# Kernel optimization log

Measured on AMD Instinct MI355X. Metric: run time of the kernel, lower is better.

Reference implementation:

```python
import jax, jax.numpy as jnp
import numpy as np

H, DK, DIM, DFF, DEPTH = 8, 64, 512, 2048, 8
B, LS, LT, VOCAB = 16, 128, 128, 32000


def setup_inputs() -> dict:
    key = jax.random.key(0)
    ks = jax.random.split(key, 20)
    w = lambda k, s: jax.random.normal(k, s, jnp.float32) * 0.02
    N_enc, N_dec = B * LS, B * LT
    base_s = np.arange(B) * LS
    base_t = np.arange(B) * LT
    i = np.arange(LS)
    j = np.arange(LT)
    # encoder self-attn: full bipartite within each sentence
    ee_src = (base_s[:, None, None] + i[None, :, None] + 0 * i[None, None, :]).reshape(-1)
    ee_dst = (base_s[:, None, None] + 0 * i[None, :, None] + i[None, None, :]).reshape(-1)
    # decoder self-attn: causal (key pos <= query pos)
    ii, jj = np.meshgrid(j, j, indexing='ij')  # ii = dst(query) pos, jj = src(key) pos
    m = jj <= ii
    dd_src = (base_t[:, None] + jj[m][None, :]).reshape(-1)
    dd_dst = (base_t[:, None] + ii[m][None, :]).reshape(-1)
    # cross-attn: enc node -> dec node, full within sentence
    ed_src = (base_s[:, None, None] + i[None, :, None] + 0 * j[None, None, :]).reshape(-1)
    ed_dst = (base_t[:, None, None] + 0 * i[None, :, None] + j[None, None, :]).reshape(-1)
    return {
        'emb_src': w(ks[0], (VOCAB, DIM)), 'emb_tgt': w(ks[1], (VOCAB, DIM)),
        'pos_emb': w(ks[2], (LS, DIM)), 'time_emb': w(ks[3], (DEPTH, DIM)),
        'Wqkv_e': w(ks[4], (DIM, 3 * DIM)), 'Wo_e': w(ks[5], (DIM, DIM)),
        'W1_e': w(ks[6], (DIM, DFF)), 'W2_e': w(ks[7], (DFF, DIM)),
        'Wqkv_d': w(ks[8], (DIM, 3 * DIM)), 'Wo_d': w(ks[9], (DIM, DIM)),
        'W1_d': w(ks[10], (DIM, DFF)), 'W2_d': w(ks[11], (DFF, DIM)),
        'Wq_x': w(ks[12], (DIM, DIM)), 'Wkv_x': w(ks[13], (DIM, 2 * DIM)),
        'Wo_x': w(ks[14], (DIM, DIM)), 'Wgen': w(ks[15], (DIM, VOCAB)),
        'src_tokens': jax.random.randint(ks[16], (N_enc,), 0, VOCAB, jnp.int32),
        'tgt_tokens': jax.random.randint(ks[17], (N_dec,), 0, VOCAB, jnp.int32),
        'src_pos': jnp.tile(jnp.arange(LS, dtype=jnp.int32), B),
        'tgt_pos': jnp.tile(jnp.arange(LT, dtype=jnp.int32), B),
        'ee_src': jnp.asarray(ee_src, jnp.int32), 'ee_dst': jnp.asarray(ee_dst, jnp.int32),
        'dd_src': jnp.asarray(dd_src, jnp.int32), 'dd_dst': jnp.asarray(dd_dst, jnp.int32),
        'ed_src': jnp.asarray(ed_src, jnp.int32), 'ed_dst': jnp.asarray(ed_dst, jnp.int32),
    }


def _ln(x):
    m = x.mean(-1, keepdims=True)
    v = ((x - m) ** 2).mean(-1, keepdims=True)
    return (x - m) * jax.lax.rsqrt(v + 1e-5)


def _attn(q, k, v, src, dst, n_dst):
    # q: [Nq,H,DK] (dst side), k/v: [Nk,H,DK] (src side); edge lists [E]
    # src_dot_dst -> scaled_exp -> scatter-sum (src_mul_edge + sum, copy_edge + sum), then wv/z
    s = jnp.exp(jnp.einsum('ehd,ehd->eh', k[src], q[dst]) / np.float32(np.sqrt(DK)))  # [E,H]
    wv = jax.ops.segment_sum(s[:, :, None] * v[src], dst, num_segments=n_dst)  # [Nq,H,DK]
    z = jax.ops.segment_sum(s, dst, num_segments=n_dst)  # [Nq,H]
    return (wv / (z[:, :, None] + 1e-9)).reshape(n_dst, DIM)


def reference(emb_src, emb_tgt, pos_emb, time_emb, Wqkv_e, Wo_e, W1_e, W2_e,
              Wqkv_d, Wo_d, W1_d, W2_d, Wq_x, Wkv_x, Wo_x, Wgen,
              src_tokens, tgt_tokens, src_pos, tgt_pos,
              ee_src, ee_dst, dd_src, dd_dst, ed_src, ed_dst):
    Ne, Nd = src_tokens.shape[0], tgt_tokens.shape[0]
    x_e = emb_src[src_tokens] + pos_emb[src_pos]
    x_d = emb_tgt[tgt_tokens] + pos_emb[tgt_pos]
    # encoder: MAX_DEPTH shared-weight iterations with time+pos enc re-added each step
    for t in range(DEPTH):
        xp = x_e + pos_emb[src_pos] + time_emb[t]
        q, k, v = jnp.split(xp @ Wqkv_e, 3, axis=-1)
        o = _attn(q.reshape(Ne, H, DK), k.reshape(Ne, H, DK), v.reshape(Ne, H, DK), ee_src, ee_dst, Ne)
        x_e = _ln(x_e + o @ Wo_e)
        x_e = _ln(x_e + jax.nn.relu(x_e @ W1_e) @ W2_e)
    # decoder: self-attn (causal dd) then cross-attn (ed) each iteration
    for t in range(DEPTH):
        xp = x_d + pos_emb[tgt_pos] + time_emb[t]
        q, k, v = jnp.split(xp @ Wqkv_d, 3, axis=-1)
        o = _attn(q.reshape(Nd, H, DK), k.reshape(Nd, H, DK), v.reshape(Nd, H, DK), dd_src, dd_dst, Nd)
        x_d = _ln(x_d + o @ Wo_d)
        qx = ((x_d + pos_emb[tgt_pos] + time_emb[t]) @ Wq_x).reshape(Nd, H, DK)
        kx, vx = jnp.split(x_e @ Wkv_x, 2, axis=-1)
        o = _attn(qx, kx.reshape(Ne, H, DK), vx.reshape(Ne, H, DK), ed_src, ed_dst, Nd)
        x_d = _ln(x_d + o @ Wo_x)
        x_d = _ln(x_d + jax.nn.relu(x_d @ W1_d) @ W2_d)
    return jax.nn.log_softmax(x_d @ Wgen, axis=-1)  # generator over dec nodes
```

## Files before the change

kernel.cpp:

```cpp
#include <hip/hip_runtime.h>
#include <hip/hip_bf16.h>
#include <math.h>

#define H 8
#define DK 64
#define DIM 512
#define DFF 2048
#define DEPTH 8
#define VOCAB 32000
#define NTOK 2048

typedef float f32x4 __attribute__((ext_vector_type(4)));
typedef short bf16x8 __attribute__((ext_vector_type(8)));

static __device__ __forceinline__ unsigned short f2bf(float f) {
    unsigned u = __float_as_uint(f);
    return (unsigned short)((u + 0x7FFFu + ((u >> 16) & 1u)) >> 16);
}

#define GLL(src, dst) __builtin_amdgcn_global_load_lds( \
    (const __attribute__((address_space(1))) unsigned int*)(src), \
    (__attribute__((address_space(3))) unsigned int*)(dst), 16, 0, 0)

static __device__ __forceinline__ void load_ln_stats(
    const float* __restrict__ stats, int base, int rows,
    float* Lm, float* Li, int tid, int nthr)
{
    for (int r = tid; r < rows; r += nthr) {
        float m = 0.f, inv = 1.f;
        if (stats) {
            const float* s = stats + (size_t)(base + r) * 16;
            float sum = 0.f, sq = 0.f;
#pragma unroll
            for (int b = 0; b < 8; b++) { sum += s[b * 2]; sq += s[b * 2 + 1]; }
            m = sum * (1.f / 512.f);
            float v = sq * (1.f / 512.f) - m * m;
            inv = 1.f / sqrtf(v + 1e-5f);
        }
        Lm[r] = m; Li[r] = inv;
    }
}

__global__ void embed_kernel(const float* __restrict__ emb, const int* __restrict__ tok,
                             const float* __restrict__ pos, const int* __restrict__ pidx,
                             float* __restrict__ out, int n4) {
    int idx = blockIdx.x * blockDim.x + threadIdx.x;
    if (idx >= n4) return;
    int i = idx >> 7, d = idx & 127;
    float4 a = ((const float4*)emb)[(size_t)tok[i] * 128 + d];
    float4 b = ((const float4*)pos)[(size_t)pidx[i] * 128 + d];
    ((float4*)out)[idx] = make_float4(a.x + b.x, a.y + b.y, a.z + b.z, a.w + b.w);
}

struct WD { const float* src; unsigned short* dst; int K; int N; int t0; int pad; };
struct WTab { WD d[12]; };

__global__ __launch_bounds__(256) void wconv_all(WTab tab) {
    __shared__ float t[32][33];
    const int bid = blockIdx.x;
    int w = 0;
#pragma unroll
    for (int i = 1; i < 12; i++) if (bid >= tab.d[i].t0) w = i;
    const float* W = tab.d[w].src;
    unsigned short* Wt = tab.d[w].dst;
    const int K = tab.d[w].K, N = tab.d[w].N;
    const int lt = bid - tab.d[w].t0;
    const int txc = N >> 5;
    const int n0 = (lt % txc) << 5, k0 = (lt / txc) << 5;
    const int tid = threadIdx.x;
    const int tx = tid & 31, ty = tid >> 5;
#pragma unroll
    for (int i = 0; i < 32; i += 8)
        t[ty + i][tx] = W[(size_t)(k0 + ty + i) * N + n0 + tx];
    __syncthreads();
#pragma unroll
    for (int i = 0; i < 32; i += 8)
        Wt[(size_t)(n0 + ty + i) * K + k0 + tx] = f2bf(t[tx][ty + i]);
}

template<int EPI>
__global__ __launch_bounds__(256) void gemm_rb(
    const float* __restrict__ Tf,
    const float* __restrict__ stats,
    const unsigned short* __restrict__ Bt,
    unsigned short* __restrict__ Cb,
    int M, int N, int K)
{
    constexpr int BN = 64, JN = 2;
    __shared__ __align__(16) unsigned short Asm[2][128 * 64];
    __shared__ __align__(16) unsigned short Bsm[2][BN * 64];
    __shared__ float Lm[128], Li[128];
    const int tid = threadIdx.x;
    const int lane = tid & 63, wid = tid >> 6;
    const int m0 = blockIdx.y * 128, n0 = blockIdx.x * BN;
    const int wm = (wid >> 1) * 64, wn = (wid & 1) * (BN / 2);
    const int NK = K >> 6;

    float4 ar0[4], ar1[4];
    auto loadA = [&](int k0) {
#pragma unroll
        for (int it = 0; it < 4; it++) {
            int q = it * 256 + tid;
            int row = q >> 3;
            int cs = q & 7;
            const float* s = Tf + (size_t)(m0 + row) * K + k0 + cs * 8;
            ar0[it] = *(const float4*)s;
            ar1[it] = *(const float4*)(s + 4);
        }
    };
    auto storeA = [&](int buf) {
#pragma unroll
        for (int it = 0; it < 4; it++) {
            int q = it * 256 + tid;
            int row = q >> 3;
            int cs = q & 7;
            float m = Lm[row], iv = Li[row];
            unsigned short c8[8];
            c8[0] = f2bf((ar0[it].x - m) * iv); c8[1] = f2bf((ar0[it].y - m) * iv);
            c8[2] = f2bf((ar0[it].z - m) * iv); c8[3] = f2bf((ar0[it].w - m) * iv);
            c8[4] = f2bf((ar1[it].x - m) * iv); c8[5] = f2bf((ar1[it].y - m) * iv);
            c8[6] = f2bf((ar1[it].z - m) * iv); c8[7] = f2bf((ar1[it].w - m) * iv);
            *(bf16x8*)&Asm[buf][row * 64 + ((cs ^ (row & 7)) * 8)] = *(bf16x8*)c8;
        }
    };
    auto stageB = [&](int k0, int buf) {
#pragma unroll
        for (int it = 0; it < BN / 32; it++) {
            int q = it * 256 + tid;
            int row = q >> 3;
            int cs = (q & 7) ^ (row & 7);
            GLL(Bt + (size_t)(n0 + row) * K + k0 + cs * 8, &Bsm[buf][q * 8]);
        }
    };

    load_ln_stats(stats, m0, 128, Lm, Li, tid, 256);
    loadA(0);
    __syncthreads();
    storeA(0);
    stageB(0, 0);

    f32x4 acc[4][JN];
#pragma unroll
    for (int i = 0; i < 4; i++)
#pragma unroll
        for (int j = 0; j < JN; j++) acc[i][j] = (f32x4){0.f, 0.f, 0.f, 0.f};

    for (int kt = 0; kt < NK; kt++) {
        __syncthreads();
        const int cur = kt & 1, nxt = (kt + 1) & 1;
        if (kt + 1 < NK) {
            stageB((kt + 1) << 6, nxt);
            loadA((kt + 1) << 6);
        }
#pragma unroll
        for (int kk = 0; kk < 2; kk++) {
            bf16x8 af[4], bfr[JN];
#pragma unroll
            for (int i = 0; i < 4; i++) {
                int rowA = wm + i * 16 + (lane & 15);
                int ca = (kk * 4 + (lane >> 4)) ^ (rowA & 7);
                af[i] = *(const bf16x8*)&Asm[cur][rowA * 64 + ca * 8];
            }
#pragma unroll
            for (int j = 0; j < JN; j++) {
                int rowB = wn + j * 16 + (lane & 15);
                int cb = (kk * 4 + (lane >> 4)) ^ (rowB & 7);
                bfr[j] = *(const bf16x8*)&Bsm[cur][rowB * 64 + cb * 8];
            }
#pragma unroll
            for (int i = 0; i < 4; i++)
#pragma unroll
                for (int j = 0; j < JN; j++)
                    acc[i][j] = __builtin_amdgcn_mfma_f32_16x16x32_bf16(af[i], bfr[j], acc[i][j], 0, 0, 0);
        }
        if (kt + 1 < NK) storeA(nxt);
    }
#pragma unroll
    for (int i = 0; i < 4; i++)
#pragma unroll
        for (int j = 0; j < JN; j++)
#pragma unroll
            for (int r = 0; r < 4; r++) {
                int row = m0 + wm + i * 16 + (lane >> 4) * 4 + r;
                int col = n0 + wn + j * 16 + (lane & 15);
                size_t idx = (size_t)row * N + col;
                float v = acc[i][j][r];
                if (EPI == 1) Cb[idx] = f2bf(fmaxf(v, 0.f));
                if (EPI == 3) Cb[idx] = f2bf(v);
            }
}

__global__ __launch_bounds__(256) void gemm_bb(
    const unsigned short* __restrict__ A,
    const unsigned short* __restrict__ Bt,
    const float* __restrict__ Tin,
    const float* __restrict__ statsIn,
    float* __restrict__ Tout,
    float* __restrict__ statsOut,
    int M, int K)
{
    __shared__ __align__(16) unsigned short Asm[2][32 * 64];
    __shared__ __align__(16) unsigned short Bsm[2][64 * 64];
    __shared__ float Lm[32], Li[32];
    __shared__ float sredS[4][32], sredQ[4][32];
    const int tid = threadIdx.x;
    const int lane = tid & 63, wid = tid >> 6;
    const int nb = blockIdx.x;
    const int m0 = blockIdx.y * 32, n0 = nb * 64;
    const int wn = wid * 16;
    const int NK = K >> 6;

    auto stage = [&](int k0, int buf) {
        {
            int q = tid;
            int row = q >> 3;
            int cs = (q & 7) ^ (row & 7);
            GLL(A + (size_t)(m0 + row) * K + k0 + cs * 8, &Asm[buf][q * 8]);
        }
#pragma unroll
        for (int it = 0; it < 2; it++) {
            int q = it * 256 + tid;
            int row = q >> 3;
            int cs = (q & 7) ^ (row & 7);
            GLL(Bt + (size_t)(n0 + row) * K + k0 + cs * 8, &Bsm[buf][q * 8]);
        }
    };

    load_ln_stats(statsIn, m0, 32, Lm, Li, tid, 256);
    stage(0, 0);

    f32x4 acc[2];
#pragma unroll
    for (int i = 0; i < 2; i++) acc[i] = (f32x4){0.f, 0.f, 0.f, 0.f};

    for (int kt = 0; kt < NK; kt++) {
        __syncthreads();
        const int cur = kt & 1, nxt = (kt + 1) & 1;
        if (kt + 1 < NK) stage((kt + 1) << 6, nxt);
#pragma unroll
        for (int kd = 0; kd < 2; kd++) {
            int rowB = wn + (lane & 15);
            int cb = (kd * 4 + (lane >> 4)) ^ (rowB & 7);
            bf16x8 bfr = *(const bf16x8*)&Bsm[cur][rowB * 64 + cb * 8];
#pragma unroll
            for (int i = 0; i < 2; i++) {
                int rowA = i * 16 + (lane & 15);
                int ca = (kd * 4 + (lane >> 4)) ^ (rowA & 7);
                bf16x8 af = *(const bf16x8*)&Asm[cur][rowA * 64 + ca * 8];
                acc[i] = __builtin_amdgcn_mfma_f32_16x16x32_bf16(af, bfr, acc[i], 0, 0, 0);
            }
        }
    }
#pragma unroll
    for (int i = 0; i < 2; i++) {
#pragma unroll
        for (int r = 0; r < 4; r++) {
            int rl = i * 16 + (lane >> 4) * 4 + r;
            int row = m0 + rl;
            int col = n0 + wn + (lane & 15);
            size_t idx = (size_t)row * DIM + col;
            float rv = (Tin[idx] - Lm[rl]) * Li[rl];
            float v = acc[i][r] + rv;
            Tout[idx] = v;
            float s = v, q = v * v;
            s += __shfl_xor(s, 1); s += __shfl_xor(s, 2);
            s += __shfl_xor(s, 4); s += __shfl_xor(s, 8);
            q += __shfl_xor(q, 1); q += __shfl_xor(q, 2);
            q += __shfl_xor(q, 4); q += __shfl_xor(q, 8);
            if ((lane & 15) == 0) { sredS[wid][rl] = s; sredQ[wid][rl] = q; }
        }
    }
    __syncthreads();
    if (tid < 32) {
        int row = tid;
        float s = sredS[0][row] + sredS[1][row] + sredS[2][row] + sredS[3][row];
        float q = sredQ[0][row] + sredQ[1][row] + sredQ[2][row] + sredQ[3][row];
        statsOut[(size_t)(m0 + row) * 16 + nb * 2] = s;
        statsOut[(size_t)(m0 + row) * 16 + nb * 2 + 1] = q;
    }
}

template<int CAUSAL>
static __device__ __forceinline__ void attn_phase2_split(
    const unsigned short* Qs, const unsigned short* Ks, const unsigned short* Vt,
    unsigned short* Psw, float* dumpf,
    int qh, int wid, int lane, int tok0, int h,
    unsigned short* __restrict__ O)
{
    const int qg = wid & 3, kh = wid >> 2;
    bf16x8 qa[2];
#pragma unroll
    for (int kd = 0; kd < 2; kd++) {
        int qr = qg * 16 + (lane & 15);
        int ch = (kd * 4 + (lane >> 4)) ^ (qr & 7);
        qa[kd] = *(const bf16x8*)&Qs[qr * 64 + ch * 8];
    }
    int jn, kcn;
    if (!CAUSAL)      { jn = 4; kcn = 2; }
    else if (kh > qh) { jn = 0; kcn = 0; }
    else if (kh < qh) { jn = 4; kcn = 2; }
    else              { kcn = (qg >> 1) + 1; jn = kcn * 2; }

    float zr[4] = {0.f, 0.f, 0.f, 0.f};
    f32x4 oacc[4];
#pragma unroll
    for (int dt = 0; dt < 4; dt++) oacc[dt] = (f32x4){0.f, 0.f, 0.f, 0.f};

    if (jn > 0) {
        f32x4 sacc[4];
#pragma unroll
        for (int j = 0; j < 4; j++) sacc[j] = (f32x4){0.f, 0.f, 0.f, 0.f};
#pragma unroll 2
        for (int kd = 0; kd < 2; kd++) {
            for (int jj = 0; jj < jn; jj++) {
                int kr = kh * 64 + jj * 16 + (lane & 15);
                int ch = (kd * 4 + (lane >> 4)) ^ (kr & 7);
                bf16x8 kf = *(const bf16x8*)&Ks[kr * 64 + ch * 8];
                sacc[jj] = __builtin_amdgcn_mfma_f32_16x16x32_bf16(qa[kd], kf, sacc[jj], 0, 0, 0);
            }
        }
        int qbase = qh * 64 + qg * 16 + (lane >> 4) * 4;
        for (int jj = 0; jj < jn; jj++) {
            int kcol = kh * 64 + jj * 16 + (lane & 15);
#pragma unroll
            for (int rr = 0; rr < 4; rr++) {
                float p = __expf(sacc[jj][rr] * 0.125f);
                if (CAUSAL && kcol > qbase + rr) p = 0.f;
                zr[rr] += p;
                int prow = (lane >> 4) * 4 + rr;
                int ch = ((jj * 2 + ((lane & 15) >> 3)) ^ (prow & 7));
                Psw[prow * 64 + ch * 8 + (lane & 7)] = f2bf(p);
            }
        }
        for (int kcl = 0; kcl < kcn; kcl++) {
            bf16x8 pa;
            {
                int prow = lane & 15;
                int ch = (kcl * 4 + (lane >> 4)) ^ (prow & 7);
                pa = *(const bf16x8*)&Psw[prow * 64 + ch * 8];
            }
            int kcg = kh * 2 + kcl;
#pragma unroll
            for (int dt = 0; dt < 4; dt++) {
                int d = dt * 16 + (lane & 15);
                bf16x8 vf = *(const bf16x8*)&Vt[d * 132 + (kcg * 4 + (lane >> 4)) * 8];
                oacc[dt] = __builtin_amdgcn_mfma_f32_16x16x32_bf16(pa, vf, oacc[dt], 0, 0, 0);
            }
        }
    }
    __syncthreads();
    if (kh == 1) {
        float* dst = dumpf + (size_t)(qg * 64 + lane) * 20;
#pragma unroll
        for (int dt = 0; dt < 4; dt++)
#pragma unroll
            for (int rr = 0; rr < 4; rr++) dst[dt * 4 + rr] = oacc[dt][rr];
#pragma unroll
        for (int rr = 0; rr < 4; rr++) dst[16 + rr] = zr[rr];
    }
    __syncthreads();
    if (kh == 0) {
        const float* src = dumpf + (size_t)(qg * 64 + lane) * 20;
#pragma unroll
        for (int dt = 0; dt < 4; dt++)
#pragma unroll
            for (int rr = 0; rr < 4; rr++) oacc[dt][rr] += src[dt * 4 + rr];
#pragma unroll
        for (int rr = 0; rr < 4; rr++) {
            float z = zr[rr] + src[16 + rr];
            z += __shfl_xor(z, 1); z += __shfl_xor(z, 2);
            z += __shfl_xor(z, 4); z += __shfl_xor(z, 8);
            zr[rr] = 1.f / (z + 1e-9f);
        }
#pragma unroll
        for (int dt = 0; dt < 4; dt++)
#pragma unroll
            for (int rr = 0; rr < 4; rr++) {
                int qrow = tok0 + qh * 64 + qg * 16 + (lane >> 4) * 4 + rr;
                O[(size_t)qrow * DIM + h * 64 + dt * 16 + (lane & 15)] =
                    f2bf(oacc[dt][rr] * zr[rr]);
            }
    }
}

template<int CAUSAL>
__global__ __launch_bounds__(512) void fused_attn(
    const float* __restrict__ Tf,
    const float* __restrict__ stats,
    const float* __restrict__ pos,
    const float* __restrict__ trow,
    const unsigned short* __restrict__ WqkvT,
    unsigned short* __restrict__ O)
{
    __shared__ __align__(16) unsigned short smem[28928];
    __shared__ float LmA[128], LiA[128];
    unsigned short* Asm = smem;
    unsigned short* Bsm = smem + 8192;
    unsigned short* Qs  = smem;
    unsigned short* Ks  = smem + 4096;
    unsigned short* Vt  = smem + 12288;
    float* dumpf = (float*)smem;
    const int tid = threadIdx.x;
    const int lane = tid & 63, wid = tid >> 6;
    unsigned short* Psw = smem + 20736 + wid * 1024;
    const int blk = blockIdx.x;
    const int qh = blk & 1, h = (blk >> 1) & 7, b = blk >> 4;
    const int tok0 = b * 128;
    const int wr = wid * 16;

    load_ln_stats(stats, tok0, 128, LmA, LiA, tid, 512);
    __syncthreads();

    f32x4 acc[12];
#pragma unroll
    for (int c = 0; c < 12; c++) acc[c] = (f32x4){0.f, 0.f, 0.f, 0.f};

    for (int k0 = 0; k0 < 512; k0 += 64) {
        if (k0) __syncthreads();
#pragma unroll
        for (int it = 0; it < 3; it++) {
            int q = it * 512 + wid * 64 + lane;
            int r = q >> 3;
            int cs = (q & 7) ^ (r & 7);
            int srow = (r < 64) ? (h * 64 + r)
                     : (r < 128) ? (512 + h * 64 + (r - 64))
                                 : (1024 + h * 64 + (r - 128));
            GLL(WqkvT + (size_t)srow * 512 + k0 + cs * 8, &Bsm[(it * 512 + wid * 64) * 8]);
        }
#pragma unroll
        for (int it = 0; it < 2; it++) {
            int q = it * 512 + tid;
            int row = q >> 3;
            int cs = q & 7;
            const float* s = Tf + (size_t)(tok0 + row) * 512 + k0 + cs * 8;
            const float* pp = pos + (size_t)row * 512 + k0 + cs * 8;
            const float* tt = trow + k0 + cs * 8;
            float4 u0 = *(const float4*)s, u1 = *(const float4*)(s + 4);
            float4 p0 = *(const float4*)pp, p1 = *(const float4*)(pp + 4);
            float4 t0 = *(const float4*)tt, t1 = *(const float4*)(tt + 4);
            float m = LmA[row], iv = LiA[row];
            unsigned short c8[8];
            c8[0] = f2bf((u0.x - m) * iv + p0.x + t0.x);
            c8[1] = f2bf((u0.y - m) * iv + p0.y + t0.y);
            c8[2] = f2bf((u0.z - m) * iv + p0.z + t0.z);
            c8[3] = f2bf((u0.w - m) * iv + p0.w + t0.w);
            c8[4] = f2bf((u1.x - m) * iv + p1.x + t1.x);
            c8[5] = f2bf((u1.y - m) * iv + p1.y + t1.y);
            c8[6] = f2bf((u1.z - m) * iv + p1.z + t1.z);
            c8[7] = f2bf((u1.w - m) * iv + p1.w + t1.w);
            *(bf16x8*)&Asm[row * 64 + ((cs ^ (row & 7)) * 8)] = *(bf16x8*)c8;
        }
        __syncthreads();
#pragma unroll
        for (int kk = 0; kk < 2; kk++) {
            int rowA = wr + (lane & 15);
            int ca = (kk * 4 + (lane >> 4)) ^ (rowA & 7);
            bf16x8 af = *(const bf16x8*)&Asm[rowA * 64 + ca * 8];
#pragma unroll
            for (int c = 0; c < 12; c++) {
                int rowB = c * 16 + (lane & 15);
                int cb = (kk * 4 + (lane >> 4)) ^ (rowB & 7);
                bf16x8 bfr = *(const bf16x8*)&Bsm[rowB * 64 + cb * 8];
                acc[c] = __builtin_amdgcn_mfma_f32_16x16x32_bf16(af, bfr, acc[c], 0, 0, 0);
            }
        }
    }
    __syncthreads();
#pragma unroll
    for (int c = 0; c < 12; c++)
#pragma unroll
        for (int r = 0; r < 4; r++) {
            int token = wr + (lane >> 4) * 4 + r;
            int col = (c & 3) * 16 + (lane & 15);
            unsigned short v = f2bf(acc[c][r]);
            if (c < 4) {
                int tl = token - qh * 64;
                if (tl >= 0 && tl < 64)
                    Qs[tl * 64 + (((col >> 3) ^ (tl & 7)) * 8) + (col & 7)] = v;
            } else if (c < 8) {
                Ks[token * 64 + (((col >> 3) ^ (token & 7)) * 8) + (col & 7)] = v;
            } else {
                Vt[col * 132 + token] = v;
            }
        }
    __syncthreads();
    attn_phase2_split<CAUSAL>(Qs, Ks, Vt, Psw, dumpf, qh, wid, lane, tok0, h, O);
}

__global__ __launch_bounds__(512) void fused_xattn(
    const float* __restrict__ Tf,
    const float* __restrict__ stats,
    const float* __restrict__ pos,
    const float* __restrict__ trow,
    const unsigned short* __restrict__ WqT,
    const unsigned short* __restrict__ kvx,
    unsigned short* __restrict__ O)
{
    __shared__ __align__(16) unsigned short smem[28928];
    __shared__ float LmA[64], LiA[64];
    unsigned short* Qs  = smem;
    unsigned short* Ks  = smem + 4096;
    unsigned short* Vt  = smem + 12288;
    unsigned short* Asm = smem + 20736;
    unsigned short* Bsm = smem + 24832;
    float* dumpf = (float*)smem;
    const int tid = threadIdx.x;
    const int lane = tid & 63, wid = tid >> 6;
    unsigned short* Psw = smem + 20736 + wid * 1024;
    const int blk = blockIdx.x;
    const int qh = blk & 1, h = (blk >> 1) & 7, b = blk >> 4;
    const int tok0 = b * 128;

    load_ln_stats(stats, tok0 + qh * 64, 64, LmA, LiA, tid, 512);

    if (wid >= 4) {
        int st = tid - 256;
        int r = st >> 1, c0 = (st & 1) * 4;
        const unsigned short* Kg = kvx + (size_t)(tok0 + r) * 1024 + h * 64;
        const unsigned short* Vg = Kg + 512;
#pragma unroll
        for (int c = c0; c < c0 + 4; c++) {
            bf16x8 kv = *(const bf16x8*)&Kg[c * 8];
            *(bf16x8*)&Ks[r * 64 + ((c ^ (r & 7)) * 8)] = kv;
            bf16x8 vv = *(const bf16x8*)&Vg[c * 8];
#pragma unroll
            for (int j = 0; j < 8; j++)
                Vt[(c * 8 + j) * 132 + r] = (unsigned short)vv[j];
        }
    }
    __syncthreads();

    f32x4 acc[4];
#pragma unroll
    for (int c = 0; c < 4; c++) acc[c] = (f32x4){0.f, 0.f, 0.f, 0.f};

    for (int k0 = 0; k0 < 512; k0 += 64) {
        if (k0) __syncthreads();
        if (tid < 256) {
#pragma unroll
            for (int it = 0; it < 2; it++) {
                int q = it * 256 + tid;
                int r = q >> 3;
                int cs = (q & 7) ^ (r & 7);
                GLL(WqT + (size_t)(h * 64 + r) * 512 + k0 + cs * 8, &Bsm[q * 8]);
            }
#pragma unroll
            for (int it = 0; it < 2; it++) {
                int q = it * 256 + tid;
                int row = q >> 3;
                int cs = q & 7;
                const float* s = Tf + (size_t)(tok0 + qh * 64 + row) * 512 + k0 + cs * 8;
                const float* pp = pos + (size_t)(qh * 64 + row) * 512 + k0 + cs * 8;
                const float* tt = trow + k0 + cs * 8;
                float4 u0 = *(const float4*)s, u1 = *(const float4*)(s + 4);
                float4 p0 = *(const float4*)pp, p1 = *(const float4*)(pp + 4);
                float4 t0 = *(const float4*)tt, t1 = *(const float4*)(tt + 4);
                float m = LmA[row], iv = LiA[row];
                unsigned short c8[8];
                c8[0] = f2bf((u0.x - m) * iv + p0.x + t0.x);
                c8[1] = f2bf((u0.y - m) * iv + p0.y + t0.y);
                c8[2] = f2bf((u0.z - m) * iv + p0.z + t0.z);
                c8[3] = f2bf((u0.w - m) * iv + p0.w + t0.w);
                c8[4] = f2bf((u1.x - m) * iv + p1.x + t1.x);
                c8[5] = f2bf((u1.y - m) * iv + p1.y + t1.y);
                c8[6] = f2bf((u1.z - m) * iv + p1.z + t1.z);
                c8[7] = f2bf((u1.w - m) * iv + p1.w + t1.w);
                *(bf16x8*)&Asm[row * 64 + ((cs ^ (row & 7)) * 8)] = *(bf16x8*)c8;
            }
        }
        __syncthreads();
        if (wid < 4) {
#pragma unroll
            for (int kk = 0; kk < 2; kk++) {
                int rowA = wid * 16 + (lane & 15);
                int ca = (kk * 4 + (lane >> 4)) ^ (rowA & 7);
                bf16x8 af = *(const bf16x8*)&Asm[rowA * 64 + ca * 8];
#pragma unroll
                for (int c = 0; c < 4; c++) {
                    int rowB = c * 16 + (lane & 15);
                    int cb = (kk * 4 + (lane >> 4)) ^ (rowB & 7);
                    bf16x8 bfr = *(const bf16x8*)&Bsm[rowB * 64 + cb * 8];
                    acc[c] = __builtin_amdgcn_mfma_f32_16x16x32_bf16(af, bfr, acc[c], 0, 0, 0);
                }
            }
        }
    }
    __syncthreads();
    if (wid < 4) {
#pragma unroll
        for (int c = 0; c < 4; c++)
#pragma unroll
            for (int r = 0; r < 4; r++) {
                int tl = wid * 16 + (lane >> 4) * 4 + r;
                int col = c * 16 + (lane & 15);
                Qs[tl * 64 + (((col >> 3) ^ (tl & 7)) * 8) + (col & 7)] = f2bf(acc[c][r]);
            }
    }
    __syncthreads();
    attn_phase2_split<0>(Qs, Ks, Vt, Psw, dumpf, qh, wid, lane, tok0, h, O);
}

__global__ __launch_bounds__(64) void ln_fin(const float* __restrict__ T,
                                             const float* __restrict__ stats,
                                             unsigned short* __restrict__ outb) {
    const int row = blockIdx.x, lane = threadIdx.x;
    const float* st = stats + (size_t)row * 16;
    float sum = 0.f, sq = 0.f;
#pragma unroll
    for (int b = 0; b < 8; b++) { sum += st[b * 2]; sq += st[b * 2 + 1]; }
    float m = sum * (1.f / 512.f);
    float v = sq * (1.f / 512.f) - m * m;
    float inv = 1.f / sqrtf(v + 1e-5f);
    const float* p = T + (size_t)row * DIM;
    unsigned short* qb = outb + (size_t)row * DIM;
#pragma unroll
    for (int i = 0; i < 8; i++)
        qb[lane + i * 64] = f2bf((p[lane + i * 64] - m) * inv);
}

template<int PASS>
__global__ __launch_bounds__(512) void gemm_gen(
    const unsigned short* __restrict__ Ab,
    const unsigned short* __restrict__ Bt,
    float* __restrict__ Out,
    float* __restrict__ pm,
    float* __restrict__ psum,
    const float* __restrict__ lse)
{
    __shared__ __align__(16) unsigned short Asm[256 * 64];
    __shared__ __align__(16) unsigned short Bsm[128 * 64];
    __shared__ float pml[8][64];
    __shared__ float psl[8][64];
    __shared__ float lsh[256];
    const int tid = threadIdx.x;
    const int lane = tid & 63, wid = tid >> 6;
    const int d = blockIdx.x + blockIdx.y * 8;
    const int t = (d & 7) * 250 + (d >> 3);
    const int mt = t & 7, nt = t >> 3;
    const int m0 = mt * 256, n0 = nt * 128;
    const int wm = (wid >> 1) * 64, wn = (wid & 1) * 64;

    if (PASS == 1) {
        for (int r = tid; r < 256; r += 512) lsh[r] = lse[m0 + r];
        __syncthreads();
    }

    f32x4 acc[4][4];
#pragma unroll
    for (int i = 0; i < 4; i++)
#pragma unroll
        for (int j = 0; j < 4; j++) acc[i][j] = (f32x4){0.f, 0.f, 0.f, 0.f};

    for (int k0 = 0; k0 < 512; k0 += 64) {
        if (k0 || PASS == 1) __syncthreads();
#pragma unroll
        for (int it = 0; it < 2; it++) {
            int q = it * 512 + tid;
            int row = q >> 3;
            int cs = (q & 7) ^ (row & 7);
            GLL(Bt + (size_t)(n0 + row) * 512 + k0 + cs * 8, &Bsm[(it * 512 + wid * 64) * 8]);
        }
#pragma unroll
        for (int it = 0; it < 4; it++) {
            int q = it * 512 + tid;
            int row = q >> 3;
            int cs = (q & 7) ^ (row & 7);
            GLL(Ab + (size_t)(m0 + row) * 512 + k0 + cs * 8, &Asm[(it * 512 + wid * 64) * 8]);
        }
        __syncthreads();
#pragma unroll
        for (int kk = 0; kk < 2; kk++) {
            bf16x8 af[4], bfr[4];
#pragma unroll
            for (int i = 0; i < 4; i++) {
                int rowA = wm + i * 16 + (lane & 15);
                int ca = (kk * 4 + (lane >> 4)) ^ (rowA & 7);
                af[i] = *(const bf16x8*)&Asm[rowA * 64 + ca * 8];
                int rowB = wn + i * 16 + (lane & 15);
                int cb = (kk * 4 + (lane >> 4)) ^ (rowB & 7);
                bfr[i] = *(const bf16x8*)&Bsm[rowB * 64 + cb * 8];
            }
#pragma unroll
            for (int i = 0; i < 4; i++)
#pragma unroll
                for (int j = 0; j < 4; j++)
                    acc[i][j] = __builtin_amdgcn_mfma_f32_16x16x32_bf16(af[i], bfr[j], acc[i][j], 0, 0, 0);
        }
    }
    if (PASS == 0) {
#pragma unroll
        for (int i = 0; i < 4; i++) {
#pragma unroll
            for (int r = 0; r < 4; r++) {
                float mx = fmaxf(fmaxf(acc[i][0][r], acc[i][1][r]),
                                 fmaxf(acc[i][2][r], acc[i][3][r]));
                mx = fmaxf(mx, __shfl_xor(mx, 1));
                mx = fmaxf(mx, __shfl_xor(mx, 2));
                mx = fmaxf(mx, __shfl_xor(mx, 4));
                mx = fmaxf(mx, __shfl_xor(mx, 8));
                float s = __expf(acc[i][0][r] - mx) + __expf(acc[i][1][r] - mx) +
                          __expf(acc[i][2][r] - mx) + __expf(acc[i][3][r] - mx);
                s += __shfl_xor(s, 1); s += __shfl_xor(s, 2);
                s += __shfl_xor(s, 4); s += __shfl_xor(s, 8);
                if ((lane & 15) == 0) {
                    int li = i * 16 + (lane >> 4) * 4 + r;
                    pml[wid][li] = mx;
                    psl[wid][li] = s;
                }
            }
        }
        __syncthreads();
        if (tid < 256) {
            int g = tid >> 6, lr = tid & 63;
            int wa = g * 2, wb = g * 2 + 1;
            float m = fmaxf(pml[wa][lr], pml[wb][lr]);
            float s = psl[wa][lr] * __expf(pml[wa][lr] - m) + psl[wb][lr] * __expf(pml[wb][lr] - m);
            pm[(size_t)(m0 + g * 64 + lr) * 256 + nt] = m;
            psum[(size_t)(m0 + g * 64 + lr) * 256 + nt] = s;
        }
    } else {
#pragma unroll
        for (int i = 0; i < 4; i++)
#pragma unroll
            for (int j = 0; j < 4; j++)
#pragma unroll
                for (int r = 0; r < 4; r++) {
                    int rl = wm + i * 16 + (lane >> 4) * 4 + r;
                    int col = n0 + wn + j * 16 + (lane & 15);
                    Out[(size_t)(m0 + rl) * VOCAB + col] = acc[i][j][r] - lsh[rl];
                }
    }
}

__global__ __launch_bounds__(64) void lse_kernel(const float* __restrict__ pm,
                                                 const float* __restrict__ psum,
                                                 float* __restrict__ lse) {
    const int row = blockIdx.x, t = threadIdx.x;
    float m = -1e30f, s = 0.f;
    for (int nb = t; nb < 250; nb += 64) {
        float mm = pm[(size_t)row * 256 + nb];
        float ss = psum[(size_t)row * 256 + nb];
        float M = fmaxf(m, mm);
        s = s * __expf(m - M) + ss * __expf(mm - M);
        m = M;
    }
#pragma unroll
    for (int off = 32; off > 0; off >>= 1) {
        float mo = __shfl_xor(m, off), so = __shfl_xor(s, off);
        float M = fmaxf(m, mo);
        s = s * __expf(m - M) + so * __expf(mo - M);
        m = M;
    }
    if (t == 0) lse[row] = m + __logf(s);
}

extern "C" void kernel_launch(void* const* d_in, const int* in_sizes, int n_in,
                              void* d_out, int out_size, void* d_ws, size_t ws_size,
                              hipStream_t stream) {
    const float* emb_src  = (const float*)d_in[0];
    const float* emb_tgt  = (const float*)d_in[1];
    const float* pos_emb  = (const float*)d_in[2];
    const float* time_emb = (const float*)d_in[3];
    const float* Wqkv_e   = (const float*)d_in[4];
    const float* Wo_e     = (const float*)d_in[5];
    const float* W1_e     = (const float*)d_in[6];
    const float* W2_e     = (const float*)d_in[7];
    const float* Wqkv_d   = (const float*)d_in[8];
    const float* Wo_d     = (const float*)d_in[9];
    const float* W1_d     = (const float*)d_in[10];
    const float* W2_d     = (const float*)d_in[11];
    const float* Wq_x     = (const float*)d_in[12];
    const float* Wkv_x    = (const float*)d_in[13];
    const float* Wo_x     = (const float*)d_in[14];
    const float* Wgen     = (const float*)d_in[15];
    const int* src_tokens = (const int*)d_in[16];
    const int* tgt_tokens = (const int*)d_in[17];
    const int* src_pos    = (const int*)d_in[18];
    const int* tgt_pos    = (const int*)d_in[19];

    char* w = (char*)d_ws;
    float* T_e0 = (float*)(w);
    float* T_e1 = (float*)(w + (4u << 20));
    float* T_d0 = (float*)(w + (8u << 20));
    float* T_d1 = (float*)(w + (12u << 20));
    float* T_d2 = (float*)(w + (16u << 20));
    unsigned short* kvx_bf = (unsigned short*)(w + (20u << 20));
    unsigned short* o_bf   = (unsigned short*)(w + (24u << 20));
    unsigned short* hid_bf = (unsigned short*)(w + (26u << 20));
    unsigned short* xd_bf  = (unsigned short*)(w + (34u << 20));
    float* pm   = (float*)(w + (36u << 20));
    float* psum = (float*)(w + (38u << 20));
    float* se0  = (float*)(w + (40u << 20));
    float* se1  = se0 + 32768;
    float* sd0  = se1 + 32768;
    float* sd1  = sd0 + 32768;
    float* sd2  = sd1 + 32768;
    float* lse  = sd2 + 32768;
    unsigned short* wts = (unsigned short*)(w + (41u << 20));

    unsigned short* WqkvE_t = wts;
    unsigned short* WoE_t   = WqkvE_t + 786432;
    unsigned short* W1E_t   = WoE_t   + 262144;
    unsigned short* W2E_t   = W1E_t   + 1048576;
    unsigned short* WqkvD_t = W2E_t   + 1048576;
    unsigned short* WoD_t   = WqkvD_t + 786432;
    unsigned short* W1D_t   = WoD_t   + 262144;
    unsigned short* W2D_t   = W1D_t   + 1048576;
    unsigned short* WqX_t   = W2D_t   + 1048576;
    unsigned short* WkvX_t  = WqX_t   + 262144;
    unsigned short* WoX_t   = WkvX_t  + 524288;
    unsigned short* Wgen_t  = WoX_t   + 262144;

    float* out = (float*)d_out;

    WTab tab;
    auto set = [&](int i, const float* s, unsigned short* d, int K, int N, int t0) {
        tab.d[i].src = s; tab.d[i].dst = d; tab.d[i].K = K; tab.d[i].N = N;
        tab.d[i].t0 = t0; tab.d[i].pad = 0;
    };
    set(0,  Wqkv_e, WqkvE_t, 512, 1536, 0);
    set(1,  Wo_e,   WoE_t,   512, 512,  768);
    set(2,  W1_e,   W1E_t,   512, 2048, 1024);
    set(3,  W2_e,   W2E_t,   2048, 512, 2048);
    set(4,  Wqkv_d, WqkvD_t, 512, 1536, 3072);
    set(5,  Wo_d,   WoD_t,   512, 512,  3840);
    set(6,  W1_d,   W1D_t,   512, 2048, 4096);
    set(7,  W2_d,   W2D_t,   2048, 512, 5120);
    set(8,  Wq_x,   WqX_t,   512, 512,  6144);
    set(9,  Wkv_x,  WkvX_t,  512, 1024, 6400);
    set(10, Wo_x,   WoX_t,   512, 512,  6912);
    set(11, Wgen,   Wgen_t,  512, 32000, 7168);
    wconv_all<<<23168, 256, 0, stream>>>(tab);

    const int n4 = NTOK * (DIM / 4);
    dim3 eb(256), eg((n4 + 255) / 256);
    embed_kernel<<<eg, eb, 0, stream>>>(emb_src, src_tokens, pos_emb, src_pos, T_e0, n4);
    embed_kernel<<<eg, eb, 0, stream>>>(emb_tgt, tgt_tokens, pos_emb, tgt_pos, T_d0, n4);

    const dim3 gFF(DFF / 64, NTOK / 128),
               gKV(1024 / 64, NTOK / 128),
               gBB(8, NTOK / 32);

    {
        const float* scur = nullptr;
        for (int t = 0; t < DEPTH; t++) {
            const float* trow = time_emb + (size_t)t * DIM;
            fused_attn<0><<<256, 512, 0, stream>>>(T_e0, scur, pos_emb, trow, WqkvE_t, o_bf);
            gemm_bb<<<gBB, 256, 0, stream>>>(o_bf, WoE_t, T_e0, scur, T_e1, se0, NTOK, 512);
            gemm_rb<1><<<gFF, 256, 0, stream>>>(T_e1, se0, W1E_t, hid_bf, NTOK, DFF, 512);
            gemm_bb<<<gBB, 256, 0, stream>>>(hid_bf, W2E_t, T_e1, se0, T_e0, se1, NTOK, 2048);
            scur = se1;
        }
    }

    gemm_rb<3><<<gKV, 256, 0, stream>>>(T_e0, se1, WkvX_t, kvx_bf, NTOK, 1024, 512);

    {
        const float* scur = nullptr;
        for (int t = 0; t < DEPTH; t++) {
            const float* trow = time_emb + (size_t)t * DIM;
            fused_attn<1><<<256, 512, 0, stream>>>(T_d0, scur, pos_emb, trow, WqkvD_t, o_bf);
            gemm_bb<<<gBB, 256, 0, stream>>>(o_bf, WoD_t, T_d0, scur, T_d1, sd0, NTOK, 512);

            fused_xattn<<<256, 512, 0, stream>>>(T_d1, sd0, pos_emb, trow, WqX_t, kvx_bf, o_bf);
            gemm_bb<<<gBB, 256, 0, stream>>>(o_bf, WoX_t, T_d1, sd0, T_d2, sd1, NTOK, 512);

            gemm_rb<1><<<gFF, 256, 0, stream>>>(T_d2, sd1, W1D_t, hid_bf, NTOK, DFF, 512);
            gemm_bb<<<gBB, 256, 0, stream>>>(hid_bf, W2D_t, T_d2, sd1, T_d0, sd2, NTOK, 2048);
            scur = sd2;
        }
    }

    ln_fin<<<NTOK, 64, 0, stream>>>(T_d0, sd2, xd_bf);
    gemm_gen<0><<<dim3(8, 250), 512, 0, stream>>>(xd_bf, Wgen_t, nullptr, pm, psum, nullptr);
    lse_kernel<<<NTOK, 64, 0, stream>>>(pm, psum, lse);
    gemm_gen<1><<<dim3(8, 250), 512, 0, stream>>>(xd_bf, Wgen_t, out, nullptr, nullptr, lse);
}
```

Measured before the change: 1.688 ms.

## Register-prefetch next A tile across MFMA loop; skip unused Q columns

Three GEMM kernels (fused self-attention QKV, cross-attention Q, and the generator GEMM) now load the next K-slice of the A operand into registers while the current slice is used for MFMAs. The registers are written to LDS at the start of the next iteration, which hides global load latency behind compute. In the QKV kernel, waves whose token rows fall outside the block's query half also skip the Q column tiles (cmin=4). That inner loop is no longer unrolled, which may cost scheduling quality and adds register pressure. The generator kernel replaces async global_load_lds for A with register staging, which raises VGPR use and may lower occupancy.

Result: slower. 2.936 ms (+74.0%).

```diff
diff --git a/kernel.cpp b/kernel.cpp
--- a/kernel.cpp
+++ b/kernel.cpp
@@ -407,7 +407,45 @@
     const int qh = blk & 1, h = (blk >> 1) & 7, b = blk >> 4;
     const int tok0 = b * 128;
     const int wr = wid * 16;
-
+    const int cmin = ((wid >> 2) == qh) ? 0 : 4;
+
+    float4 ua[2], ub[2];
+    auto loadT = [&](int k0) {
+#pragma unroll
+        for (int it = 0; it < 2; it++) {
+            int q = it * 512 + tid;
+            int row = q >> 3;
+            int cs = q & 7;
+            const float* s = Tf + (size_t)(tok0 + row) * 512 + k0 + cs * 8;
+            ua[it] = *(const float4*)s;
+            ub[it] = *(const float4*)(s + 4);
+        }
+    };
+    auto storeT = [&](int k0) {
+#pragma unroll
+        for (int it = 0; it < 2; it++) {
+            int q = it * 512 + tid;
+            int row = q >> 3;
+            int cs = q & 7;
+            const float* pp = pos + (size_t)row * 512 + k0 + cs * 8;
+            const float* tt = trow + k0 + cs * 8;
+            float4 p0 = *(const float4*)pp, p1 = *(const float4*)(pp + 4);
+            float4 t0 = *(const float4*)tt, t1 = *(const float4*)(tt + 4);
+            float m = LmA[row], iv = LiA[row];
+            unsigned short c8[8];
+            c8[0] = f2bf((ua[it].x - m) * iv + p0.x + t0.x);
+            c8[1] = f2bf((ua[it].y - m) * iv + p0.y + t0.y);
+            c8[2] = f2bf((ua[it].z - m) * iv + p0.z + t0.z);
+            c8[3] = f2bf((ua[it].w - m) * iv + p0.w + t0.w);
+            c8[4] = f2bf((ub[it].x - m) * iv + p1.x + t1.x);
+            c8[5] = f2bf((ub[it].y - m) * iv + p1.y + t1.y);
+            c8[6] = f2bf((ub[it].z - m) * iv + p1.z + t1.z);
+            c8[7] = f2bf((ub[it].w - m) * iv + p1.w + t1.w);
+            *(bf16x8*)&Asm[row * 64 + ((cs ^ (row & 7)) * 8)] = *(bf16x8*)c8;
+        }
+    };
+
+    loadT(0);
     load_ln_stats(stats, tok0, 128, LmA, LiA, tid, 512);
     __syncthreads();
 
@@ -417,6 +455,7 @@
 
     for (int k0 = 0; k0 < 512; k0 += 64) {
         if (k0) __syncthreads();
+        storeT(k0);
 #pragma unroll
         for (int it = 0; it < 3; it++) {
             int q = it * 512 + wid * 64 + lane;
@@ -427,37 +466,14 @@
                                  : (1024 + h * 64 + (r - 128));
             GLL(WqkvT + (size_t)srow * 512 + k0 + cs * 8, &Bsm[(it * 512 + wid * 64) * 8]);
         }
-#pragma unroll
-        for (int it = 0; it < 2; it++) {
-            int q = it * 512 + tid;
-            int row = q >> 3;
-            int cs = q & 7;
-            const float* s = Tf + (size_t)(tok0 + row) * 512 + k0 + cs * 8;
-            const float* pp = pos + (size_t)row * 512 + k0 + cs * 8;
-            const float* tt = trow + k0 + cs * 8;
-            float4 u0 = *(const float4*)s, u1 = *(const float4*)(s + 4);
-            float4 p0 = *(const float4*)pp, p1 = *(const float4*)(pp + 4);
-            float4 t0 = *(const float4*)tt, t1 = *(const float4*)(tt + 4);
-            float m = LmA[row], iv = LiA[row];
-            unsigned short c8[8];
-            c8[0] = f2bf((u0.x - m) * iv + p0.x + t0.x);
-            c8[1] = f2bf((u0.y - m) * iv + p0.y + t0.y);
-            c8[2] = f2bf((u0.z - m) * iv + p0.z + t0.z);
-            c8[3] = f2bf((u0.w - m) * iv + p0.w + t0.w);
-            c8[4] = f2bf((u1.x - m) * iv + p1.x + t1.x);
-            c8[5] = f2bf((u1.y - m) * iv + p1.y + t1.y);
-            c8[6] = f2bf((u1.z - m) * iv + p1.z + t1.z);
-            c8[7] = f2bf((u1.w - m) * iv + p1.w + t1.w);
-            *(bf16x8*)&Asm[row * 64 + ((cs ^ (row & 7)) * 8)] = *(bf16x8*)c8;
-        }
         __syncthreads();
+        if (k0 + 64 < 512) loadT(k0 + 64);
 #pragma unroll
         for (int kk = 0; kk < 2; kk++) {
             int rowA = wr + (lane & 15);
             int ca = (kk * 4 + (lane >> 4)) ^ (rowA & 7);
             bf16x8 af = *(const bf16x8*)&Asm[rowA * 64 + ca * 8];
-#pragma unroll
-            for (int c = 0; c < 12; c++) {
+            for (int c = cmin; c < 12; c++) {
                 int rowB = c * 16 + (lane & 15);
                 int cb = (kk * 4 + (lane >> 4)) ^ (rowB & 7);
                 bf16x8 bfr = *(const bf16x8*)&Bsm[rowB * 64 + cb * 8];
@@ -511,6 +527,43 @@
     const int qh = blk & 1, h = (blk >> 1) & 7, b = blk >> 4;
     const int tok0 = b * 128;
 
+    float4 ua[2], ub[2];
+    auto loadT = [&](int k0) {
+#pragma unroll
+        for (int it = 0; it < 2; it++) {
+            int q = it * 256 + tid;
+            int row = q >> 3;
+            int cs = q & 7;
+            const float* s = Tf + (size_t)(tok0 + qh * 64 + row) * 512 + k0 + cs * 8;
+            ua[it] = *(const float4*)s;
+            ub[it] = *(const float4*)(s + 4);
+        }
+    };
+    auto storeT = [&](int k0) {
+#pragma unroll
+        for (int it = 0; it < 2; it++) {
+            int q = it * 256 + tid;
+            int row = q >> 3;
+            int cs = q & 7;
+            const float* pp = pos + (size_t)(qh * 64 + row) * 512 + k0 + cs * 8;
+            const float* tt = trow + k0 + cs * 8;
+            float4 p0 = *(const float4*)pp, p1 = *(const float4*)(pp + 4);
+            float4 t0 = *(const float4*)tt, t1 = *(const float4*)(tt + 4);
+            float m = LmA[row], iv = LiA[row];
+            unsigned short c8[8];
+            c8[0] = f2bf((ua[it].x - m) * iv + p0.x + t0.x);
+            c8[1] = f2bf((ua[it].y - m) * iv + p0.y + t0.y);
+            c8[2] = f2bf((ua[it].z - m) * iv + p0.z + t0.z);
+            c8[3] = f2bf((ua[it].w - m) * iv + p0.w + t0.w);
+            c8[4] = f2bf((ub[it].x - m) * iv + p1.x + t1.x);
+            c8[5] = f2bf((ub[it].y - m) * iv + p1.y + t1.y);
+            c8[6] = f2bf((ub[it].z - m) * iv + p1.z + t1.z);
+            c8[7] = f2bf((ub[it].w - m) * iv + p1.w + t1.w);
+            *(bf16x8*)&Asm[row * 64 + ((cs ^ (row & 7)) * 8)] = *(bf16x8*)c8;
+        }
+    };
+
+    if (tid < 256) loadT(0);
     load_ln_stats(stats, tok0 + qh * 64, 64, LmA, LiA, tid, 512);
 
     if (wid >= 4) {
@@ -537,6 +590,7 @@
     for (int k0 = 0; k0 < 512; k0 += 64) {
         if (k0) __syncthreads();
         if (tid < 256) {
+            storeT(k0);
 #pragma unroll
             for (int it = 0; it < 2; it++) {
                 int q = it * 256 + tid;
@@ -544,31 +598,9 @@
                 int cs = (q & 7) ^ (r & 7);
                 GLL(WqT + (size_t)(h * 64 + r) * 512 + k0 + cs * 8, &Bsm[q * 8]);
             }
-#pragma unroll
-            for (int it = 0; it < 2; it++) {
-                int q = it * 256 + tid;
-                int row = q >> 3;
-                int cs = q & 7;
-                const float* s = Tf + (size_t)(tok0 + qh * 64 + row) * 512 + k0 + cs * 8;
-                const float* pp = pos + (size_t)(qh * 64 + row) * 512 + k0 + cs * 8;
-                const float* tt = trow + k0 + cs * 8;
-                float4 u0 = *(const float4*)s, u1 = *(const float4*)(s + 4);
-                float4 p0 = *(const float4*)pp, p1 = *(const float4*)(pp + 4);
-                float4 t0 = *(const float4*)tt, t1 = *(const float4*)(tt + 4);
-                float m = LmA[row], iv = LiA[row];
-                unsigned short c8[8];
-                c8[0] = f2bf((u0.x - m) * iv + p0.x + t0.x);
-                c8[1] = f2bf((u0.y - m) * iv + p0.y + t0.y);
-                c8[2] = f2bf((u0.z - m) * iv + p0.z + t0.z);
-                c8[3] = f2bf((u0.w - m) * iv + p0.w + t0.w);
-                c8[4] = f2bf((u1.x - m) * iv + p1.x + t1.x);
-                c8[5] = f2bf((u1.y - m) * iv + p1.y + t1.y);
-                c8[6] = f2bf((u1.z - m) * iv + p1.z + t1.z);
-                c8[7] = f2bf((u1.w - m) * iv + p1.w + t1.w);
-                *(bf16x8*)&Asm[row * 64 + ((cs ^ (row & 7)) * 8)] = *(bf16x8*)c8;
-            }
         }
         __syncthreads();
+        if (tid < 256 && k0 + 64 < 512) loadT(k0 + 64);
         if (wid < 4) {
 #pragma unroll
             for (int kk = 0; kk < 2; kk++) {
@@ -640,10 +672,31 @@
     const int m0 = mt * 256, n0 = nt * 128;
     const int wm = (wid >> 1) * 64, wn = (wid & 1) * 64;
 
+    bf16x8 ar[4];
+    auto loadA = [&](int k0) {
+#pragma unroll
+        for (int it = 0; it < 4; it++) {
+            int q = it * 512 + tid;
+            int row = q >> 3;
+            int cs = q & 7;
+            ar[it] = *(const bf16x8*)&Ab[(size_t)(m0 + row) * 512 + k0 + cs * 8];
+        }
+    };
+    auto storeA = [&]() {
+#pragma unroll
+        for (int it = 0; it < 4; it++) {
+            int q = it * 512 + tid;
+            int row = q >> 3;
+            int cs = q & 7;
+            *(bf16x8*)&Asm[row * 64 + ((cs ^ (row & 7)) * 8)] = ar[it];
+        }
+    };
+
     if (PASS == 1) {
         for (int r = tid; r < 256; r += 512) lsh[r] = lse[m0 + r];
-        __syncthreads();
-    }
+    }
+    loadA(0);
+    if (PASS == 1) __syncthreads();
 
     f32x4 acc[4][4];
 #pragma unroll
@@ -652,7 +705,8 @@
         for (int j = 0; j < 4; j++) acc[i][j] = (f32x4){0.f, 0.f, 0.f, 0.f};
 
     for (int k0 = 0; k0 < 512; k0 += 64) {
-        if (k0 || PASS == 1) __syncthreads();
+        if (k0) __syncthreads();
+        storeA();
 #pragma unroll
         for (int it = 0; it < 2; it++) {
             int q = it * 512 + tid;
@@ -660,14 +714,8 @@
             int cs = (q & 7) ^ (row & 7);
             GLL(Bt + (size_t)(n0 + row) * 512 + k0 + cs * 8, &Bsm[(it * 512 + wid * 64) * 8]);
         }
-#pragma unroll
-        for (int it = 0; it < 4; it++) {
-            int q = it * 512 + tid;
-            int row = q >> 3;
-            int cs = (q & 7) ^ (row & 7);
-            GLL(Ab + (size_t)(m0 + row) * 512 + k0 + cs * 8, &Asm[(it * 512 + wid * 64) * 8]);
-        }
         __syncthreads();
+        if (k0 + 64 < 512) loadA(k0 + 64);
 #pragma unroll
         for (int kk = 0; kk < 2; kk++) {
             bf16x8 af[4], bfr[4];
```
